# Kernel optimization log

Hardware: AMD Instinct MI355X
Metric: run time of the kernel (lower is better)

Reference implementation:

```python
import jax, jax.numpy as jnp
import numpy as np

B, T, C, HD = 4, 2048, 1024, 64

def setup_inputs() -> dict:
    key = jax.random.key(0)
    kx, kq, kk, kv = jax.random.split(key, 4)
    # Weights stored as [n_embed, head_size]; equivalent to torch Linear weight transposed.
    scale = 1.0 / np.sqrt(C)
    return {
        "x": jax.random.normal(kx, (B, T, C), dtype=jnp.float32),
        "Wq": jax.random.normal(kq, (C, HD), dtype=jnp.float32) * scale,
        "Wk": jax.random.normal(kk, (C, HD), dtype=jnp.float32) * scale,
        "Wv": jax.random.normal(kv, (C, HD), dtype=jnp.float32) * scale,
    }

def reference(x, Wq, Wk, Wv):
    # Projections (no bias)
    q = x @ Wq  # [B,T,HD]
    k = x @ Wk
    v = x @ Wv
    hd = k.shape[-1]
    # NOTE: original multiplies by sqrt(head_size) (not the usual 1/sqrt) -- faithful.
    scores = jnp.einsum("btd,bsd->bts", q, k) * (hd ** 0.5)  # [B,T,T]
    # First softmax over full (unmasked) rows
    w = jax.nn.softmax(scores, axis=-1)
    # Causal mask applied AFTER the first softmax, then a second softmax
    causal = jnp.tril(jnp.ones((q.shape[1], q.shape[1]), dtype=bool))  # [T,T]
    w = jnp.where(causal[None, :, :], w, -jnp.inf)
    w = jax.nn.softmax(w, axis=-1)
    out = jnp.einsum("bts,bsd->btd", w, v)  # [B,T,HD]
    return out
```

## Files before the change

### kernel.cpp

```cpp
#include <hip/hip_runtime.h>
#include <math.h>

#define T_  2048
#define C_  1024
#define HD_ 64

typedef __attribute__((ext_vector_type(8))) short bf16x8;
typedef __attribute__((ext_vector_type(4))) float f32x4;

#define MFMA_BF16(A, B, C) __builtin_amdgcn_mfma_f32_16x16x32_bf16(A, B, C, 0, 0, 0)

__device__ __forceinline__ short f2bf(float f) {
    union { float f; unsigned u; } v; v.f = f;
    unsigned r = v.u + 0x7fffu + ((v.u >> 16) & 1u);
    return (short)(r >> 16);
}
__device__ __forceinline__ float bf2f(short s) {
    union { float f; unsigned u; } v;
    v.u = ((unsigned)(unsigned short)s) << 16;
    return v.f;
}

__global__ __launch_bounds__(256) void prep_w_kernel(
    const float* __restrict__ Wq, const float* __restrict__ Wk,
    const float* __restrict__ Wv, short* __restrict__ wt)
{
    const int m = blockIdx.y;
    const float* W = (m == 0) ? Wq : (m == 1) ? Wk : Wv;
    const int t = threadIdx.x;
    const int c = blockIdx.x * 64 + (t >> 2);
    const int hg = (t & 3) * 16;
    const float4* wp = (const float4*)(W + (size_t)c * HD_ + hg);
    short* hi = wt + (size_t)(m * 2 + 0) * 64 * 1024;
    short* lo = wt + (size_t)(m * 2 + 1) * 64 * 1024;
    #pragma unroll
    for (int u = 0; u < 4; ++u) {
        float4 f = wp[u];
        float vs[4] = {f.x, f.y, f.z, f.w};
        #pragma unroll
        for (int e = 0; e < 4; ++e) {
            int h = hg + u * 4 + e;
            short hh = f2bf(vs[e]);
            hi[(size_t)h * 1024 + c] = hh;
            lo[(size_t)h * 1024 + c] = f2bf(vs[e] - bf2f(hh));
        }
    }
}

__global__ __launch_bounds__(256) void qkv_proj_kernel(
    const float* __restrict__ x, const short* __restrict__ wt,
    short* __restrict__ qhp, short* __restrict__ qlp,
    short* __restrict__ khp, short* __restrict__ klp,
    short* __restrict__ vtp)
{
    __shared__ __align__(16) short xh[32 * 64], xl[32 * 64];
    __shared__ __align__(16) short wh[192 * 64], wl[192 * 64];

    const int t = threadIdx.x, L = t & 63, wv = t >> 6;
    const int R0 = blockIdx.x * 32;
    const int xrow = t >> 3, xch = t & 7;

    f32x4 acc[2][3];
    #pragma unroll
    for (int i = 0; i < 2; ++i)
        #pragma unroll
        for (int j = 0; j < 3; ++j) acc[i][j] = {0.f, 0.f, 0.f, 0.f};

    float4 xa0, xa1;
    bf16x8 wr[2][6];
    const float* xp = x + (size_t)(R0 + xrow) * C_ + xch * 8;

    auto loadX = [&](int c0) {
        xa0 = *(const float4*)(xp + c0);
        xa1 = *(const float4*)(xp + c0 + 4);
    };
    auto loadW = [&](int c0) {
        #pragma unroll
        for (int pl = 0; pl < 2; ++pl)
            #pragma unroll
            for (int u = 0; u < 6; ++u) {
                int cc = t + 256 * u;
                int row = cc >> 3, ch = cc & 7;
                int m = row >> 6, h = row & 63;
                wr[pl][u] = *(const bf16x8*)(wt + (size_t)(m * 2 + pl) * 65536
                                             + (size_t)h * 1024 + c0 + ch * 8);
            }
    };

    loadX(0); loadW(0);
    for (int c0 = 0; c0 < C_; c0 += 64) {
        __syncthreads();
        {
            float vs[8] = {xa0.x, xa0.y, xa0.z, xa0.w, xa1.x, xa1.y, xa1.z, xa1.w};
            bf16x8 vh, vl;
            #pragma unroll
            for (int e = 0; e < 8; ++e) {
                short hh = f2bf(vs[e]);
                vh[e] = hh;
                vl[e] = f2bf(vs[e] - bf2f(hh));
            }
            int slot = (xch ^ (xrow & 7)) * 8;
            *(bf16x8*)&xh[xrow * 64 + slot] = vh;
            *(bf16x8*)&xl[xrow * 64 + slot] = vl;
        }
        {
            #pragma unroll
            for (int pl = 0; pl < 2; ++pl)
                #pragma unroll
                for (int u = 0; u < 6; ++u) {
                    int cc = t + 256 * u;
                    int row = cc >> 3, ch = cc & 7;
                    short* dst = pl ? wl : wh;
                    *(bf16x8*)&dst[row * 64 + ((ch ^ (row & 7)) * 8)] = wr[pl][u];
                }
        }
        if (c0 + 64 < C_) { loadX(c0 + 64); loadW(c0 + 64); }
        __syncthreads();
        #pragma unroll
        for (int kc = 0; kc < 2; ++kc) {
            const int ch = kc * 4 + (L >> 4);
            bf16x8 axh[2], axl[2], bwh[3], bwl[3];
            #pragma unroll
            for (int rt = 0; rt < 2; ++rt) {
                int row = rt * 16 + (L & 15);
                int off = row * 64 + ((ch ^ (row & 7)) * 8);
                axh[rt] = *(const bf16x8*)&xh[off];
                axl[rt] = *(const bf16x8*)&xl[off];
            }
            #pragma unroll
            for (int cl = 0; cl < 3; ++cl) {
                int ct = wv + cl * 4;
                int wrow = ct * 16 + (L & 15);
                int off = wrow * 64 + ((ch ^ (wrow & 7)) * 8);
                bwh[cl] = *(const bf16x8*)&wh[off];
                bwl[cl] = *(const bf16x8*)&wl[off];
            }
            #pragma unroll
            for (int rt = 0; rt < 2; ++rt) {
                acc[rt][0] = MFMA_BF16(axl[rt], bwh[0], acc[rt][0]);
                acc[rt][0] = MFMA_BF16(axh[rt], bwl[0], acc[rt][0]);
                acc[rt][0] = MFMA_BF16(axh[rt], bwh[0], acc[rt][0]);
                acc[rt][1] = MFMA_BF16(axl[rt], bwh[1], acc[rt][1]);
                acc[rt][1] = MFMA_BF16(axh[rt], bwl[1], acc[rt][1]);
                acc[rt][1] = MFMA_BF16(axh[rt], bwh[1], acc[rt][1]);
                acc[rt][2] = MFMA_BF16(bwh[2], axh[rt], acc[rt][2]);
            }
        }
    }

    const int quad = L >> 4;
    #pragma unroll
    for (int rt = 0; rt < 2; ++rt) {
        #pragma unroll
        for (int r = 0; r < 4; ++r) {
            int row = R0 + rt * 16 + quad * 4 + r;
            int h = wv * 16 + (L & 15);
            float vq = acc[rt][0][r] * 8.f;
            short hq = f2bf(vq);
            qhp[(size_t)row * HD_ + h] = hq;
            qlp[(size_t)row * HD_ + h] = f2bf(vq - bf2f(hq));
            float vk = acc[rt][1][r];
            short hk = f2bf(vk);
            khp[(size_t)row * HD_ + h] = hk;
            klp[(size_t)row * HD_ + h] = f2bf(vk - bf2f(hk));
            int d = wv * 16 + quad * 4 + r;
            int tt = R0 + rt * 16 + (L & 15);
            int bb = tt >> 11, tl = tt & (T_ - 1);
            vtp[(size_t)(bb * 64 + d) * T_ + tl] = f2bf(acc[rt][2][r]);
        }
    }
}

__global__ __launch_bounds__(256) void stats_kernel(
    const short* __restrict__ qhp, const short* __restrict__ qlp,
    const short* __restrict__ khp, const short* __restrict__ klp,
    float* __restrict__ pm)
{
    __shared__ __align__(16) short khs[64 * 64], kls[64 * 64];
    __shared__ float red[4 * 64 * 2];

    const int t = threadIdx.x, L = t & 63, wv = t >> 6;
    const int bt = blockIdx.x, seg = blockIdx.y, b = blockIdx.z;
    const int R0 = bt * 64, S0 = seg * 512;

    bf16x8 qfh[4][2], qfl[4][2];
    #pragma unroll
    for (int rt = 0; rt < 4; ++rt)
        #pragma unroll
        for (int dc = 0; dc < 2; ++dc) {
            int row = R0 + rt * 16 + (L & 15);
            size_t off = ((size_t)b * T_ + row) * HD_ + dc * 32 + (L >> 4) * 8;
            qfh[rt][dc] = *(const bf16x8*)(qhp + off);
            qfl[rt][dc] = *(const bf16x8*)(qlp + off);
        }

    float ml[4][4], ll[4][4];
    #pragma unroll
    for (int rt = 0; rt < 4; ++rt)
        #pragma unroll
        for (int r = 0; r < 4; ++r) { ml[rt][r] = -1e30f; ll[rt][r] = 0.f; }

    const int pl = t >> 7, id = t & 127;
    for (int jt = 0; jt < 8; ++jt) {
        __syncthreads();
        {
            const short* src = pl ? klp : khp;
            short* dst = pl ? kls : khs;
            #pragma unroll
            for (int u = 0; u < 4; ++u) {
                int cid = id * 4 + u;
                int col = cid >> 3, ch = cid & 7;
                bf16x8 v = *(const bf16x8*)(src
                    + ((size_t)b * T_ + S0 + jt * 64 + col) * HD_ + ch * 8);
                *(bf16x8*)&dst[col * 64 + ((ch ^ (col & 7)) * 8)] = v;
            }
        }
        __syncthreads();
        const int colL = wv * 16 + (L & 15);
        bf16x8 kf[2], kfl[2];
        #pragma unroll
        for (int dc = 0; dc < 2; ++dc) {
            int ch = dc * 4 + (L >> 4);
            int off = colL * 64 + ((ch ^ (colL & 7)) * 8);
            kf[dc]  = *(const bf16x8*)&khs[off];
            kfl[dc] = *(const bf16x8*)&kls[off];
        }
        #pragma unroll
        for (int rt = 0; rt < 4; ++rt) {
            f32x4 s = {0.f, 0.f, 0.f, 0.f};
            #pragma unroll
            for (int dc = 0; dc < 2; ++dc) {
                s = MFMA_BF16(qfl[rt][dc], kf[dc], s);
                s = MFMA_BF16(qfh[rt][dc], kfl[dc], s);
                s = MFMA_BF16(qfh[rt][dc], kf[dc], s);
            }
            #pragma unroll
            for (int r = 0; r < 4; ++r) {
                float mn = fmaxf(ml[rt][r], s[r]);
                ll[rt][r] = ll[rt][r] * __expf(ml[rt][r] - mn) + __expf(s[r] - mn);
                ml[rt][r] = mn;
            }
        }
    }
    #pragma unroll
    for (int off = 1; off < 16; off <<= 1)
        #pragma unroll
        for (int rt = 0; rt < 4; ++rt)
            #pragma unroll
            for (int r = 0; r < 4; ++r) {
                float mo = __shfl_xor(ml[rt][r], off, 64);
                float lo = __shfl_xor(ll[rt][r], off, 64);
                float mn = fmaxf(ml[rt][r], mo);
                ll[rt][r] = ll[rt][r] * __expf(ml[rt][r] - mn) + lo * __expf(mo - mn);
                ml[rt][r] = mn;
            }
    if ((L & 15) == 0) {
        #pragma unroll
        for (int rt = 0; rt < 4; ++rt)
            #pragma unroll
            for (int r = 0; r < 4; ++r) {
                int row = rt * 16 + (L >> 4) * 4 + r;
                red[(wv * 64 + row) * 2 + 0] = ml[rt][r];
                red[(wv * 64 + row) * 2 + 1] = ll[rt][r];
            }
    }
    __syncthreads();
    if (t < 64) {
        float M = red[t * 2], S = red[t * 2 + 1];
        #pragma unroll
        for (int w = 1; w < 4; ++w) {
            float mo = red[(w * 64 + t) * 2], lo = red[(w * 64 + t) * 2 + 1];
            float mn = fmaxf(M, mo);
            S = S * __expf(M - mn) + lo * __expf(mo - mn);
            M = mn;
        }
        size_t o = ((size_t)((b * 32 + bt) * 4 + seg) * 64 + t) * 2;
        pm[o] = M;
        pm[o + 1] = S;
    }
}

__global__ __launch_bounds__(256) void stat_merge_kernel(
    const float* __restrict__ pm, float* __restrict__ msp, float* __restrict__ ilp)
{
    int gid = blockIdx.x * 256 + threadIdx.x;
    int b = gid >> 11, rl = gid & 2047, bt = rl >> 6, rr = rl & 63;
    float M = -1e30f, S = 0.f;
    #pragma unroll
    for (int seg = 0; seg < 4; ++seg) {
        size_t o = ((size_t)((b * 32 + bt) * 4 + seg) * 64 + rr) * 2;
        float mo = pm[o], lo = pm[o + 1];
        float mn = fmaxf(M, mo);
        S = S * __expf(M - mn) + lo * __expf(mo - mn);
        M = mn;
    }
    msp[gid] = M;
    ilp[gid] = 1.f / S;
}

__global__ __launch_bounds__(512) void pv_kernel(
    const short* __restrict__ qhp, const short* __restrict__ qlp,
    const short* __restrict__ khp, const short* __restrict__ klp,
    const short* __restrict__ vtp, const float* __restrict__ msp,
    const float* __restrict__ ilp, float* __restrict__ out)
{
    __shared__ __align__(16) short khs[128 * 64];
    __shared__ __align__(16) short kls[128 * 64];
    __shared__ __align__(16) short vts[64 * 128];
    __shared__ __align__(16) float es[32 * 128];

    const int t = threadIdx.x, L = t & 63, wv = t >> 6;
    const int b = blockIdx.x >> 6, p = blockIdx.x & 63;
    const int IA = p * 16, IB = (127 - p) * 16;

    bf16x8 qfh[2][2], qfl[2][2];
    #pragma unroll
    for (int rt = 0; rt < 2; ++rt) {
        int row = (rt ? IB : IA) + (L & 15);
        const short* qb  = qhp + ((size_t)b * T_ + row) * HD_;
        const short* qbl = qlp + ((size_t)b * T_ + row) * HD_;
        #pragma unroll
        for (int dc = 0; dc < 2; ++dc) {
            int off = dc * 32 + (L >> 4) * 8;
            qfh[rt][dc] = *(const bf16x8*)(qb + off);
            qfl[rt][dc] = *(const bf16x8*)(qbl + off);
        }
    }
    float ms[2][4], is[2][4];
    int rowg[2][4];
    #pragma unroll
    for (int rt = 0; rt < 2; ++rt)
        #pragma unroll
        for (int r = 0; r < 4; ++r) {
            int rg = (rt ? IB : IA) + (L >> 4) * 4 + r;
            rowg[rt][r] = rg;
            ms[rt][r] = msp[b * T_ + rg];
            is[rt][r] = ilp[b * T_ + rg];
        }

    const short* kbh = khp + (size_t)b * T_ * HD_;
    const short* kbl = klp + (size_t)b * T_ * HD_;
    const short* vb  = vtp + (size_t)b * 64 * T_;
    const int spl = t >> 8, sid = t & 255;

    auto stageK = [&](int jt) {
        const short* src = spl ? kbl : kbh;
        short* dst = spl ? kls : khs;
        #pragma unroll
        for (int u = 0; u < 4; ++u) {
            int cid = sid * 4 + u;
            int col = cid >> 3, c8 = cid & 7;
            bf16x8 v = *(const bf16x8*)(src + (size_t)(jt * 128 + col) * HD_ + c8 * 8);
            *(bf16x8*)&dst[col * 64 + ((c8 ^ (col & 7)) * 8)] = v;
        }
    };
    auto stageV = [&](int jt) {
        #pragma unroll
        for (int u = 0; u < 2; ++u) {
            int cid = t + u * 512;
            int d = cid >> 4, ch = cid & 15;
            bf16x8 v = *(const bf16x8*)(vb + (size_t)d * T_ + jt * 128 + ch * 8);
            *(bf16x8*)&vts[d * 128 + ((ch ^ ((d & 7) * 2)) * 8)] = v;
        }
    };

    const int nA = (IA + 143) >> 7;
    const int nB = (IB + 143) >> 7;
    const int rtp = wv & 1, dh = (wv >> 1) & 1, khf = wv >> 2;
    f32x4 ov[2];
    ov[0] = {0.f, 0.f, 0.f, 0.f};
    ov[1] = {0.f, 0.f, 0.f, 0.f};
    float dn[2][4];
    #pragma unroll
    for (int rt = 0; rt < 2; ++rt)
        #pragma unroll
        for (int r = 0; r < 4; ++r) dn[rt][r] = 0.f;

    for (int jt = 0; jt < nB; ++jt) {
        __syncthreads();
        stageK(jt);
        stageV(jt);
        __syncthreads();
        const int col = wv * 16 + (L & 15);
        bf16x8 kf[2], kfl[2];
        #pragma unroll
        for (int dc = 0; dc < 2; ++dc) {
            int ch = dc * 4 + (L >> 4);
            int off = col * 64 + ((ch ^ (col & 7)) * 8);
            kf[dc]  = *(const bf16x8*)&khs[off];
            kfl[dc] = *(const bf16x8*)&kls[off];
        }
        for (int rt = 0; rt < 2; ++rt) {
            if (rt == 0 && jt >= nA) continue;
            f32x4 s = {0.f, 0.f, 0.f, 0.f};
            #pragma unroll
            for (int dc = 0; dc < 2; ++dc) {
                s = MFMA_BF16(qfl[rt][dc], kf[dc], s);
                s = MFMA_BF16(qfh[rt][dc], kfl[dc], s);
                s = MFMA_BF16(qfh[rt][dc], kf[dc], s);
            }
            #pragma unroll
            for (int r = 0; r < 4; ++r) {
                float pv = __expf(s[r] - ms[rt][r]) * is[rt][r];
                int colg = jt * 128 + col;
                float ev = (colg <= rowg[rt][r]) ? __expf(pv) : 0.f;
                dn[rt][r] += ev;
                int rid = rt * 16 + (L >> 4) * 4 + r;
                es[rid * 128 + (((col >> 3) ^ (rid & 15)) * 8) + (col & 7)] = ev;
            }
        }
        __syncthreads();
        if (!(rtp == 0 && jt >= nA)) {
            #pragma unroll
            for (int u = 0; u < 2; ++u) {
                int kc = khf * 2 + u;
                int rid = rtp * 16 + (L & 15);
                int chunk = (kc * 4 + (L >> 4)) ^ (rid & 15);
                const float* ep = &es[rid * 128 + chunk * 8];
                float4 e0 = *(const float4*)ep;
                float4 e1 = *(const float4*)(ep + 4);
                bf16x8 ef;
                ef[0] = f2bf(e0.x); ef[1] = f2bf(e0.y);
                ef[2] = f2bf(e0.z); ef[3] = f2bf(e0.w);
                ef[4] = f2bf(e1.x); ef[5] = f2bf(e1.y);
                ef[6] = f2bf(e1.z); ef[7] = f2bf(e1.w);
                #pragma unroll
                for (int dt = 0; dt < 2; ++dt) {
                    int d = dh * 32 + dt * 16 + (L & 15);
                    int ch = kc * 4 + (L >> 4);
                    bf16x8 vf = *(const bf16x8*)&vts[d * 128 + ((ch ^ ((d & 7) * 2)) * 8)];
                    ov[dt] = MFMA_BF16(ef, vf, ov[dt]);
                }
            }
        }
    }

    #pragma unroll
    for (int off = 1; off < 16; off <<= 1)
        #pragma unroll
        for (int rt = 0; rt < 2; ++rt)
            #pragma unroll
            for (int r = 0; r < 4; ++r)
                dn[rt][r] += __shfl_xor(dn[rt][r], off, 64);
    __syncthreads();
    float* red  = es + 2304;
    float* dinv = es + 2560;
    if ((L & 15) == 0) {
        #pragma unroll
        for (int rt = 0; rt < 2; ++rt)
            #pragma unroll
            for (int r = 0; r < 4; ++r) {
                int rid = rt * 16 + (L >> 4) * 4 + r;
                red[wv * 32 + rid] = dn[rt][r];
            }
    }
    __syncthreads();
    if (t < 32) {
        float D = 0.f;
        #pragma unroll
        for (int w = 0; w < 8; ++w) D += red[w * 32 + t];
        dinv[t] = 1.f / D;
    }
    float* obuf = es;
    __syncthreads();
    if (khf == 1) {
        #pragma unroll
        for (int dt = 0; dt < 2; ++dt)
            #pragma unroll
            for (int r = 0; r < 4; ++r)
                obuf[((wv - 4) * 64 + L) * 8 + dt * 4 + r] = ov[dt][r];
    }
    __syncthreads();
    if (khf == 0) {
        float* ob = out + (size_t)b * T_ * HD_;
        #pragma unroll
        for (int dt = 0; dt < 2; ++dt)
            #pragma unroll
            for (int r = 0; r < 4; ++r) {
                float o = ov[dt][r] + obuf[(wv * 64 + L) * 8 + dt * 4 + r];
                int rid = rtp * 16 + (L >> 4) * 4 + r;
                int row = (rtp ? IB : IA) + (L >> 4) * 4 + r;
                int d = dh * 32 + dt * 16 + (L & 15);
                ob[(size_t)row * HD_ + d] = o * dinv[rid];
            }
    }
}

extern "C" void kernel_launch(void* const* d_in, const int* in_sizes, int n_in,
                              void* d_out, int out_size, void* d_ws, size_t ws_size,
                              hipStream_t stream) {
    (void)in_sizes; (void)n_in; (void)out_size; (void)ws_size;
    const float* x  = (const float*)d_in[0];
    const float* Wq = (const float*)d_in[1];
    const float* Wk = (const float*)d_in[2];
    const float* Wv = (const float*)d_in[3];
    float* outp = (float*)d_out;

    char* ws = (char*)d_ws;
    short* wt  = (short*)ws;
    float* pm  = (float*)ws;
    float* msp = (float*)(ws + 262144);
    float* ilp = (float*)(ws + 294912);
    short* qh = (short*)(ws + 786432);
    short* ql = (short*)(ws + 786432 + 1048576);
    short* kh = (short*)(ws + 786432 + 2 * 1048576);
    short* kl = (short*)(ws + 786432 + 3 * 1048576);
    short* vt = (short*)(ws + 786432 + 4 * 1048576);

    prep_w_kernel<<<dim3(16, 3), 256, 0, stream>>>(Wq, Wk, Wv, wt);
    qkv_proj_kernel<<<dim3(256), 256, 0, stream>>>(x, wt, qh, ql, kh, kl, vt);
    stats_kernel<<<dim3(32, 4, 4), 256, 0, stream>>>(qh, ql, kh, kl, pm);
    stat_merge_kernel<<<dim3(32), 256, 0, stream>>>(pm, msp, ilp);
    pv_kernel<<<dim3(256), 512, 0, stream>>>(qh, ql, kh, kl, vt, msp, ilp, outp);
}
```

Baseline: 155.8 us.

## Drop LDS staging for K/V/W loads, split-K projection, fuse stats merge

Several independent changes. The weight prep now transposes through LDS so global stores are coalesced. The projection kernel goes to 512 threads, splits the reduction dimension across wave pairs and reads x and weights straight from global memory without LDS tiles, then reduces the partial sums through shared memory. The stats kernel is reorganised so each block owns 16 rows over the full key range, which removes the separate merge kernel and one launch. The pv kernel loads K and V fragments directly from global memory (relying on L2/L1) instead of staging them in swizzled LDS, and uses a padded score buffer. The risk is uncoalesced or repeated global reads in place of the LDS reuse the old code had.

```diff
diff --git a/kernel.cpp b/kernel.cpp
--- a/kernel.cpp
+++ b/kernel.cpp
@@ -25,40 +25,51 @@
     const float* __restrict__ Wq, const float* __restrict__ Wk,
     const float* __restrict__ Wv, short* __restrict__ wt)
 {
+    __shared__ __align__(16) short hi_l[64 * 72], lo_l[64 * 72];
     const int m = blockIdx.y;
     const float* W = (m == 0) ? Wq : (m == 1) ? Wk : Wv;
     const int t = threadIdx.x;
-    const int c = blockIdx.x * 64 + (t >> 2);
-    const int hg = (t & 3) * 16;
-    const float4* wp = (const float4*)(W + (size_t)c * HD_ + hg);
-    short* hi = wt + (size_t)(m * 2 + 0) * 64 * 1024;
-    short* lo = wt + (size_t)(m * 2 + 1) * 64 * 1024;
-    #pragma unroll
-    for (int u = 0; u < 4; ++u) {
-        float4 f = wp[u];
-        float vs[4] = {f.x, f.y, f.z, f.w};
-        #pragma unroll
-        for (int e = 0; e < 4; ++e) {
-            int h = hg + u * 4 + e;
-            short hh = f2bf(vs[e]);
-            hi[(size_t)h * 1024 + c] = hh;
-            lo[(size_t)h * 1024 + c] = f2bf(vs[e] - bf2f(hh));
-        }
-    }
-}
-
-__global__ __launch_bounds__(256) void qkv_proj_kernel(
+    const int C0 = blockIdx.x * 64;
+    {
+        const int c = t >> 2, hq = t & 3;
+        const float4* wp = (const float4*)(W + (size_t)(C0 + c) * HD_ + hq * 16);
+        #pragma unroll
+        for (int u = 0; u < 4; ++u) {
+            float4 f = wp[u];
+            float vs[4] = {f.x, f.y, f.z, f.w};
+            #pragma unroll
+            for (int e = 0; e < 4; ++e) {
+                int h = hq * 16 + u * 4 + e;
+                short hh = f2bf(vs[e]);
+                hi_l[h * 72 + c] = hh;
+                lo_l[h * 72 + c] = f2bf(vs[e] - bf2f(hh));
+            }
+        }
+    }
+    __syncthreads();
+    {
+        const int h = t >> 2, cc = (t & 3) * 16;
+        short* dh = wt + (size_t)(m * 2 + 0) * 65536 + h * 1024 + C0 + cc;
+        short* dl = wt + (size_t)(m * 2 + 1) * 65536 + h * 1024 + C0 + cc;
+        *(bf16x8*)dh       = *(const bf16x8*)&hi_l[h * 72 + cc];
+        *(bf16x8*)(dh + 8) = *(const bf16x8*)&hi_l[h * 72 + cc + 8];
+        *(bf16x8*)dl       = *(const bf16x8*)&lo_l[h * 72 + cc];
+        *(bf16x8*)(dl + 8) = *(const bf16x8*)&lo_l[h * 72 + cc + 8];
+    }
+}
+
+__global__ __launch_bounds__(512) void qkv_proj_kernel(
     const float* __restrict__ x, const short* __restrict__ wt,
     short* __restrict__ qhp, short* __restrict__ qlp,
     short* __restrict__ khp, short* __restrict__ klp,
     short* __restrict__ vtp)
 {
-    __shared__ __align__(16) short xh[32 * 64], xl[32 * 64];
-    __shared__ __align__(16) short wh[192 * 64], wl[192 * 64];
+    __shared__ __align__(16) float pbuf[4 * 64 * 28];
 
     const int t = threadIdx.x, L = t & 63, wv = t >> 6;
+    const int kq = wv & 1, colq = wv >> 1;
     const int R0 = blockIdx.x * 32;
-    const int xrow = t >> 3, xch = t & 7;
+    const int h = colq * 16 + (L & 15);
 
     f32x4 acc[2][3];
     #pragma unroll
@@ -66,107 +77,81 @@
         #pragma unroll
         for (int j = 0; j < 3; ++j) acc[i][j] = {0.f, 0.f, 0.f, 0.f};
 
-    float4 xa0, xa1;
-    bf16x8 wr[2][6];
-    const float* xp = x + (size_t)(R0 + xrow) * C_ + xch * 8;
-
-    auto loadX = [&](int c0) {
-        xa0 = *(const float4*)(xp + c0);
-        xa1 = *(const float4*)(xp + c0 + 4);
-    };
-    auto loadW = [&](int c0) {
-        #pragma unroll
-        for (int pl = 0; pl < 2; ++pl)
-            #pragma unroll
-            for (int u = 0; u < 6; ++u) {
-                int cc = t + 256 * u;
-                int row = cc >> 3, ch = cc & 7;
-                int m = row >> 6, h = row & 63;
-                wr[pl][u] = *(const bf16x8*)(wt + (size_t)(m * 2 + pl) * 65536
-                                             + (size_t)h * 1024 + c0 + ch * 8);
-            }
-    };
-
-    loadX(0); loadW(0);
-    for (int c0 = 0; c0 < C_; c0 += 64) {
-        __syncthreads();
-        {
-            float vs[8] = {xa0.x, xa0.y, xa0.z, xa0.w, xa1.x, xa1.y, xa1.z, xa1.w};
-            bf16x8 vh, vl;
+    const int c_base = kq * 512 + (L >> 4) * 8;
+    const float* xp0 = x + (size_t)(R0 + (L & 15)) * C_ + c_base;
+    const float* xp1 = x + (size_t)(R0 + 16 + (L & 15)) * C_ + c_base;
+    const short* wq_h = wt + (size_t)0 * 65536 + h * 1024 + c_base;
+    const short* wq_l = wt + (size_t)1 * 65536 + h * 1024 + c_base;
+    const short* wk_h = wt + (size_t)2 * 65536 + h * 1024 + c_base;
+    const short* wk_l = wt + (size_t)3 * 65536 + h * 1024 + c_base;
+    const short* wv_h = wt + (size_t)4 * 65536 + h * 1024 + c_base;
+
+    for (int it = 0; it < 16; ++it) {
+        const int c0 = it * 32;
+        bf16x8 axh[2], axl[2];
+        #pragma unroll
+        for (int rt = 0; rt < 2; ++rt) {
+            const float* xp = rt ? xp1 : xp0;
+            float4 f0 = *(const float4*)(xp + c0);
+            float4 f1 = *(const float4*)(xp + c0 + 4);
+            float vs[8] = {f0.x, f0.y, f0.z, f0.w, f1.x, f1.y, f1.z, f1.w};
             #pragma unroll
             for (int e = 0; e < 8; ++e) {
                 short hh = f2bf(vs[e]);
-                vh[e] = hh;
-                vl[e] = f2bf(vs[e] - bf2f(hh));
-            }
-            int slot = (xch ^ (xrow & 7)) * 8;
-            *(bf16x8*)&xh[xrow * 64 + slot] = vh;
-            *(bf16x8*)&xl[xrow * 64 + slot] = vl;
-        }
-        {
-            #pragma unroll
-            for (int pl = 0; pl < 2; ++pl)
-                #pragma unroll
-                for (int u = 0; u < 6; ++u) {
-                    int cc = t + 256 * u;
-                    int row = cc >> 3, ch = cc & 7;
-                    short* dst = pl ? wl : wh;
-                    *(bf16x8*)&dst[row * 64 + ((ch ^ (row & 7)) * 8)] = wr[pl][u];
-                }
-        }
-        if (c0 + 64 < C_) { loadX(c0 + 64); loadW(c0 + 64); }
-        __syncthreads();
-        #pragma unroll
-        for (int kc = 0; kc < 2; ++kc) {
-            const int ch = kc * 4 + (L >> 4);
-            bf16x8 axh[2], axl[2], bwh[3], bwl[3];
-            #pragma unroll
-            for (int rt = 0; rt < 2; ++rt) {
-                int row = rt * 16 + (L & 15);
-                int off = row * 64 + ((ch ^ (row & 7)) * 8);
-                axh[rt] = *(const bf16x8*)&xh[off];
-                axl[rt] = *(const bf16x8*)&xl[off];
-            }
-            #pragma unroll
-            for (int cl = 0; cl < 3; ++cl) {
-                int ct = wv + cl * 4;
-                int wrow = ct * 16 + (L & 15);
-                int off = wrow * 64 + ((ch ^ (wrow & 7)) * 8);
-                bwh[cl] = *(const bf16x8*)&wh[off];
-                bwl[cl] = *(const bf16x8*)&wl[off];
-            }
-            #pragma unroll
-            for (int rt = 0; rt < 2; ++rt) {
-                acc[rt][0] = MFMA_BF16(axl[rt], bwh[0], acc[rt][0]);
-                acc[rt][0] = MFMA_BF16(axh[rt], bwl[0], acc[rt][0]);
-                acc[rt][0] = MFMA_BF16(axh[rt], bwh[0], acc[rt][0]);
-                acc[rt][1] = MFMA_BF16(axl[rt], bwh[1], acc[rt][1]);
-                acc[rt][1] = MFMA_BF16(axh[rt], bwl[1], acc[rt][1]);
-                acc[rt][1] = MFMA_BF16(axh[rt], bwh[1], acc[rt][1]);
-                acc[rt][2] = MFMA_BF16(bwh[2], axh[rt], acc[rt][2]);
-            }
-        }
-    }
-
-    const int quad = L >> 4;
-    #pragma unroll
-    for (int rt = 0; rt < 2; ++rt) {
-        #pragma unroll
-        for (int r = 0; r < 4; ++r) {
-            int row = R0 + rt * 16 + quad * 4 + r;
-            int h = wv * 16 + (L & 15);
-            float vq = acc[rt][0][r] * 8.f;
-            short hq = f2bf(vq);
-            qhp[(size_t)row * HD_ + h] = hq;
-            qlp[(size_t)row * HD_ + h] = f2bf(vq - bf2f(hq));
-            float vk = acc[rt][1][r];
-            short hk = f2bf(vk);
-            khp[(size_t)row * HD_ + h] = hk;
-            klp[(size_t)row * HD_ + h] = f2bf(vk - bf2f(hk));
-            int d = wv * 16 + quad * 4 + r;
-            int tt = R0 + rt * 16 + (L & 15);
-            int bb = tt >> 11, tl = tt & (T_ - 1);
-            vtp[(size_t)(bb * 64 + d) * T_ + tl] = f2bf(acc[rt][2][r]);
+                axh[rt][e] = hh;
+                axl[rt][e] = f2bf(vs[e] - bf2f(hh));
+            }
+        }
+        bf16x8 qh_f = *(const bf16x8*)(wq_h + c0);
+        bf16x8 ql_f = *(const bf16x8*)(wq_l + c0);
+        bf16x8 kh_f = *(const bf16x8*)(wk_h + c0);
+        bf16x8 kl_f = *(const bf16x8*)(wk_l + c0);
+        bf16x8 vh_f = *(const bf16x8*)(wv_h + c0);
+        #pragma unroll
+        for (int rt = 0; rt < 2; ++rt) {
+            acc[rt][0] = MFMA_BF16(axl[rt], qh_f, acc[rt][0]);
+            acc[rt][0] = MFMA_BF16(axh[rt], ql_f, acc[rt][0]);
+            acc[rt][0] = MFMA_BF16(axh[rt], qh_f, acc[rt][0]);
+            acc[rt][1] = MFMA_BF16(axl[rt], kh_f, acc[rt][1]);
+            acc[rt][1] = MFMA_BF16(axh[rt], kl_f, acc[rt][1]);
+            acc[rt][1] = MFMA_BF16(axh[rt], kh_f, acc[rt][1]);
+            acc[rt][2] = MFMA_BF16(vh_f, axh[rt], acc[rt][2]);
+        }
+    }
+
+    if (kq == 1) {
+        float* pb = &pbuf[(colq * 64 + L) * 28];
+        #pragma unroll
+        for (int rt = 0; rt < 2; ++rt)
+            #pragma unroll
+            for (int j = 0; j < 3; ++j)
+                *(f32x4*)&pb[(rt * 3 + j) * 4] = acc[rt][j];
+    }
+    __syncthreads();
+    if (kq == 0) {
+        const float* pb = &pbuf[(colq * 64 + L) * 28];
+        const int quad = L >> 4;
+        #pragma unroll
+        for (int rt = 0; rt < 2; ++rt) {
+            f32x4 aq = acc[rt][0] + *(const f32x4*)&pb[(rt * 3 + 0) * 4];
+            f32x4 ak = acc[rt][1] + *(const f32x4*)&pb[(rt * 3 + 1) * 4];
+            f32x4 av = acc[rt][2] + *(const f32x4*)&pb[(rt * 3 + 2) * 4];
+            #pragma unroll
+            for (int r = 0; r < 4; ++r) {
+                int row = R0 + rt * 16 + quad * 4 + r;
+                float vq = aq[r] * 8.f;
+                short hq2 = f2bf(vq);
+                qhp[(size_t)row * HD_ + h] = hq2;
+                qlp[(size_t)row * HD_ + h] = f2bf(vq - bf2f(hq2));
+                float vk = ak[r];
+                short hk2 = f2bf(vk);
+                khp[(size_t)row * HD_ + h] = hk2;
+                klp[(size_t)row * HD_ + h] = f2bf(vk - bf2f(hk2));
+                int d = colq * 16 + quad * 4 + r;
+                int tt = R0 + rt * 16 + (L & 15);
+                int bb = tt >> 11, tl = tt & (T_ - 1);
+                vtp[(size_t)(bb * 64 + d) * T_ + tl] = f2bf(av[r]);
+            }
         }
     }
 }
@@ -174,128 +159,93 @@
 __global__ __launch_bounds__(256) void stats_kernel(
     const short* __restrict__ qhp, const short* __restrict__ qlp,
     const short* __restrict__ khp, const short* __restrict__ klp,
-    float* __restrict__ pm)
+    float* __restrict__ msp, float* __restrict__ ilp)
 {
-    __shared__ __align__(16) short khs[64 * 64], kls[64 * 64];
-    __shared__ float red[4 * 64 * 2];
+    __shared__ float smem[4][16][2];
 
     const int t = threadIdx.x, L = t & 63, wv = t >> 6;
-    const int bt = blockIdx.x, seg = blockIdx.y, b = blockIdx.z;
-    const int R0 = bt * 64, S0 = seg * 512;
-
-    bf16x8 qfh[4][2], qfl[4][2];
-    #pragma unroll
-    for (int rt = 0; rt < 4; ++rt)
+    const int R0 = blockIdx.x * 16;
+    const int b = R0 >> 11;
+    const int CB = (b << 11) + wv * 512;
+
+    bf16x8 qfh[2], qfl[2];
+    {
+        int row = R0 + (L & 15);
         #pragma unroll
         for (int dc = 0; dc < 2; ++dc) {
-            int row = R0 + rt * 16 + (L & 15);
-            size_t off = ((size_t)b * T_ + row) * HD_ + dc * 32 + (L >> 4) * 8;
-            qfh[rt][dc] = *(const bf16x8*)(qhp + off);
-            qfl[rt][dc] = *(const bf16x8*)(qlp + off);
-        }
-
-    float ml[4][4], ll[4][4];
-    #pragma unroll
-    for (int rt = 0; rt < 4; ++rt)
-        #pragma unroll
-        for (int r = 0; r < 4; ++r) { ml[rt][r] = -1e30f; ll[rt][r] = 0.f; }
-
-    const int pl = t >> 7, id = t & 127;
-    for (int jt = 0; jt < 8; ++jt) {
-        __syncthreads();
-        {
-            const short* src = pl ? klp : khp;
-            short* dst = pl ? kls : khs;
-            #pragma unroll
-            for (int u = 0; u < 4; ++u) {
-                int cid = id * 4 + u;
-                int col = cid >> 3, ch = cid & 7;
-                bf16x8 v = *(const bf16x8*)(src
-                    + ((size_t)b * T_ + S0 + jt * 64 + col) * HD_ + ch * 8);
-                *(bf16x8*)&dst[col * 64 + ((ch ^ (col & 7)) * 8)] = v;
-            }
-        }
-        __syncthreads();
-        const int colL = wv * 16 + (L & 15);
-        bf16x8 kf[2], kfl[2];
-        #pragma unroll
-        for (int dc = 0; dc < 2; ++dc) {
-            int ch = dc * 4 + (L >> 4);
-            int off = colL * 64 + ((ch ^ (colL & 7)) * 8);
-            kf[dc]  = *(const bf16x8*)&khs[off];
-            kfl[dc] = *(const bf16x8*)&kls[off];
-        }
-        #pragma unroll
-        for (int rt = 0; rt < 4; ++rt) {
-            f32x4 s = {0.f, 0.f, 0.f, 0.f};
-            #pragma unroll
-            for (int dc = 0; dc < 2; ++dc) {
-                s = MFMA_BF16(qfl[rt][dc], kf[dc], s);
-                s = MFMA_BF16(qfh[rt][dc], kfl[dc], s);
-                s = MFMA_BF16(qfh[rt][dc], kf[dc], s);
-            }
-            #pragma unroll
-            for (int r = 0; r < 4; ++r) {
-                float mn = fmaxf(ml[rt][r], s[r]);
-                ll[rt][r] = ll[rt][r] * __expf(ml[rt][r] - mn) + __expf(s[r] - mn);
-                ml[rt][r] = mn;
-            }
+            size_t off = (size_t)row * HD_ + dc * 32 + (L >> 4) * 8;
+            qfh[dc] = *(const bf16x8*)(qhp + off);
+            qfl[dc] = *(const bf16x8*)(qlp + off);
+        }
+    }
+
+    float M[4], S[4];
+    #pragma unroll
+    for (int r = 0; r < 4; ++r) { M[r] = -1e30f; S[r] = 0.f; }
+
+    for (int chunk = 0; chunk < 2; ++chunk) {
+        f32x4 s[16];
+        #pragma unroll
+        for (int ct = 0; ct < 16; ++ct) {
+            int col = CB + (chunk * 16 + ct) * 16 + (L & 15);
+            const short* kb  = khp + (size_t)col * HD_ + (L >> 4) * 8;
+            const short* kb2 = klp + (size_t)col * HD_ + (L >> 4) * 8;
+            bf16x8 kf0 = *(const bf16x8*)kb;
+            bf16x8 kf1 = *(const bf16x8*)(kb + 32);
+            bf16x8 kl0 = *(const bf16x8*)kb2;
+            bf16x8 kl1 = *(const bf16x8*)(kb2 + 32);
+            f32x4 a = {0.f, 0.f, 0.f, 0.f};
+            a = MFMA_BF16(qfl[0], kf0, a);
+            a = MFMA_BF16(qfh[0], kl0, a);
+            a = MFMA_BF16(qfh[0], kf0, a);
+            a = MFMA_BF16(qfl[1], kf1, a);
+            a = MFMA_BF16(qfh[1], kl1, a);
+            a = MFMA_BF16(qfh[1], kf1, a);
+            s[ct] = a;
+        }
+        #pragma unroll
+        for (int r = 0; r < 4; ++r) {
+            float mc = s[0][r];
+            #pragma unroll
+            for (int ct = 1; ct < 16; ++ct) mc = fmaxf(mc, s[ct][r]);
+            float lc = 0.f;
+            #pragma unroll
+            for (int ct = 0; ct < 16; ++ct) lc += __expf(s[ct][r] - mc);
+            float mn = fmaxf(M[r], mc);
+            S[r] = S[r] * __expf(M[r] - mn) + lc * __expf(mc - mn);
+            M[r] = mn;
         }
     }
     #pragma unroll
     for (int off = 1; off < 16; off <<= 1)
         #pragma unroll
-        for (int rt = 0; rt < 4; ++rt)
-            #pragma unroll
-            for (int r = 0; r < 4; ++r) {
-                float mo = __shfl_xor(ml[rt][r], off, 64);
-                float lo = __shfl_xor(ll[rt][r], off, 64);
-                float mn = fmaxf(ml[rt][r], mo);
-                ll[rt][r] = ll[rt][r] * __expf(ml[rt][r] - mn) + lo * __expf(mo - mn);
-                ml[rt][r] = mn;
-            }
+        for (int r = 0; r < 4; ++r) {
+            float mo = __shfl_xor(M[r], off, 64);
+            float lo = __shfl_xor(S[r], off, 64);
+            float mn = fmaxf(M[r], mo);
+            S[r] = S[r] * __expf(M[r] - mn) + lo * __expf(mo - mn);
+            M[r] = mn;
+        }
     if ((L & 15) == 0) {
         #pragma unroll
-        for (int rt = 0; rt < 4; ++rt)
-            #pragma unroll
-            for (int r = 0; r < 4; ++r) {
-                int row = rt * 16 + (L >> 4) * 4 + r;
-                red[(wv * 64 + row) * 2 + 0] = ml[rt][r];
-                red[(wv * 64 + row) * 2 + 1] = ll[rt][r];
-            }
-    }
-    __syncthreads();
-    if (t < 64) {
-        float M = red[t * 2], S = red[t * 2 + 1];
+        for (int r = 0; r < 4; ++r) {
+            smem[wv][(L >> 4) * 4 + r][0] = M[r];
+            smem[wv][(L >> 4) * 4 + r][1] = S[r];
+        }
+    }
+    __syncthreads();
+    if (t < 16) {
+        float Mm = smem[0][t][0], Ss = smem[0][t][1];
         #pragma unroll
         for (int w = 1; w < 4; ++w) {
-            float mo = red[(w * 64 + t) * 2], lo = red[(w * 64 + t) * 2 + 1];
-            float mn = fmaxf(M, mo);
-            S = S * __expf(M - mn) + lo * __expf(mo - mn);
-            M = mn;
-        }
-        size_t o = ((size_t)((b * 32 + bt) * 4 + seg) * 64 + t) * 2;
-        pm[o] = M;
-        pm[o + 1] = S;
-    }
-}
-
-__global__ __launch_bounds__(256) void stat_merge_kernel(
-    const float* __restrict__ pm, float* __restrict__ msp, float* __restrict__ ilp)
-{
-    int gid = blockIdx.x * 256 + threadIdx.x;
-    int b = gid >> 11, rl = gid & 2047, bt = rl >> 6, rr = rl & 63;
-    float M = -1e30f, S = 0.f;
-    #pragma unroll
-    for (int seg = 0; seg < 4; ++seg) {
-        size_t o = ((size_t)((b * 32 + bt) * 4 + seg) * 64 + rr) * 2;
-        float mo = pm[o], lo = pm[o + 1];
-        float mn = fmaxf(M, mo);
-        S = S * __expf(M - mn) + lo * __expf(mo - mn);
-        M = mn;
-    }
-    msp[gid] = M;
-    ilp[gid] = 1.f / S;
+            float mo = smem[w][t][0], lo = smem[w][t][1];
+            float mn = fmaxf(Mm, mo);
+            Ss = Ss * __expf(Mm - mn) + lo * __expf(mo - mn);
+            Mm = mn;
+        }
+        msp[R0 + t] = Mm;
+        ilp[R0 + t] = 1.f / Ss;
+    }
 }
 
 __global__ __launch_bounds__(512) void pv_kernel(
@@ -304,10 +254,10 @@
     const short* __restrict__ vtp, const float* __restrict__ msp,
     const float* __restrict__ ilp, float* __restrict__ out)
 {
-    __shared__ __align__(16) short khs[128 * 64];
-    __shared__ __align__(16) short kls[128 * 64];
-    __shared__ __align__(16) short vts[64 * 128];
-    __shared__ __align__(16) float es[32 * 128];
+    __shared__ __align__(16) float es[32 * 132];
+    __shared__ float red[8 * 32];
+    __shared__ float dinv[32];
+    __shared__ float obuf[4 * 64 * 8];
 
     const int t = threadIdx.x, L = t & 63, wv = t >> 6;
     const int b = blockIdx.x >> 6, p = blockIdx.x & 63;
@@ -317,8 +267,8 @@
     #pragma unroll
     for (int rt = 0; rt < 2; ++rt) {
         int row = (rt ? IB : IA) + (L & 15);
-        const short* qb  = qhp + ((size_t)b * T_ + row) * HD_;
-        const short* qbl = qlp + ((size_t)b * T_ + row) * HD_;
+        const short* qb  = qhp + ((size_t)(b << 11) + row) * HD_;
+        const short* qbl = qlp + ((size_t)(b << 11) + row) * HD_;
         #pragma unroll
         for (int dc = 0; dc < 2; ++dc) {
             int off = dc * 32 + (L >> 4) * 8;
@@ -334,35 +284,9 @@
         for (int r = 0; r < 4; ++r) {
             int rg = (rt ? IB : IA) + (L >> 4) * 4 + r;
             rowg[rt][r] = rg;
-            ms[rt][r] = msp[b * T_ + rg];
-            is[rt][r] = ilp[b * T_ + rg];
-        }
-
-    const short* kbh = khp + (size_t)b * T_ * HD_;
-    const short* kbl = klp + (size_t)b * T_ * HD_;
-    const short* vb  = vtp + (size_t)b * 64 * T_;
-    const int spl = t >> 8, sid = t & 255;
-
-    auto stageK = [&](int jt) {
-        const short* src = spl ? kbl : kbh;
-        short* dst = spl ? kls : khs;
-        #pragma unroll
-        for (int u = 0; u < 4; ++u) {
-            int cid = sid * 4 + u;
-            int col = cid >> 3, c8 = cid & 7;
-            bf16x8 v = *(const bf16x8*)(src + (size_t)(jt * 128 + col) * HD_ + c8 * 8);
-            *(bf16x8*)&dst[col * 64 + ((c8 ^ (col & 7)) * 8)] = v;
-        }
-    };
-    auto stageV = [&](int jt) {
-        #pragma unroll
-        for (int u = 0; u < 2; ++u) {
-            int cid = t + u * 512;
-            int d = cid >> 4, ch = cid & 15;
-            bf16x8 v = *(const bf16x8*)(vb + (size_t)d * T_ + jt * 128 + ch * 8);
-            *(bf16x8*)&vts[d * 128 + ((ch ^ ((d & 7) * 2)) * 8)] = v;
-        }
-    };
+            ms[rt][r] = msp[(b << 11) + rg];
+            is[rt][r] = ilp[(b << 11) + rg];
+        }
 
     const int nA = (IA + 143) >> 7;
     const int nB = (IB + 143) >> 7;
@@ -378,45 +302,40 @@
 
     for (int jt = 0; jt < nB; ++jt) {
         __syncthreads();
-        stageK(jt);
-        stageV(jt);
-        __syncthreads();
-        const int col = wv * 16 + (L & 15);
-        bf16x8 kf[2], kfl[2];
-        #pragma unroll
-        for (int dc = 0; dc < 2; ++dc) {
-            int ch = dc * 4 + (L >> 4);
-            int off = col * 64 + ((ch ^ (col & 7)) * 8);
-            kf[dc]  = *(const bf16x8*)&khs[off];
-            kfl[dc] = *(const bf16x8*)&kls[off];
-        }
+        const int colL = wv * 16 + (L & 15);
+        const int gcol = (b << 11) + jt * 128 + colL;
+        const short* kb  = khp + (size_t)gcol * HD_ + (L >> 4) * 8;
+        const short* kb2 = klp + (size_t)gcol * HD_ + (L >> 4) * 8;
+        bf16x8 kf0 = *(const bf16x8*)kb;
+        bf16x8 kf1 = *(const bf16x8*)(kb + 32);
+        bf16x8 kl0 = *(const bf16x8*)kb2;
+        bf16x8 kl1 = *(const bf16x8*)(kb2 + 32);
         for (int rt = 0; rt < 2; ++rt) {
             if (rt == 0 && jt >= nA) continue;
             f32x4 s = {0.f, 0.f, 0.f, 0.f};
-            #pragma unroll
-            for (int dc = 0; dc < 2; ++dc) {
-                s = MFMA_BF16(qfl[rt][dc], kf[dc], s);
-                s = MFMA_BF16(qfh[rt][dc], kfl[dc], s);
-                s = MFMA_BF16(qfh[rt][dc], kf[dc], s);
-            }
+            s = MFMA_BF16(qfl[rt][0], kf0, s);
+            s = MFMA_BF16(qfh[rt][0], kl0, s);
+            s = MFMA_BF16(qfh[rt][0], kf0, s);
+            s = MFMA_BF16(qfl[rt][1], kf1, s);
+            s = MFMA_BF16(qfh[rt][1], kl1, s);
+            s = MFMA_BF16(qfh[rt][1], kf1, s);
+            const int colg = jt * 128 + colL;
             #pragma unroll
             for (int r = 0; r < 4; ++r) {
                 float pv = __expf(s[r] - ms[rt][r]) * is[rt][r];
-                int colg = jt * 128 + col;
                 float ev = (colg <= rowg[rt][r]) ? __expf(pv) : 0.f;
                 dn[rt][r] += ev;
                 int rid = rt * 16 + (L >> 4) * 4 + r;
-                es[rid * 128 + (((col >> 3) ^ (rid & 15)) * 8) + (col & 7)] = ev;
+                es[rid * 132 + colL] = ev;
             }
         }
         __syncthreads();
         if (!(rtp == 0 && jt >= nA)) {
             #pragma unroll
             for (int u = 0; u < 2; ++u) {
-                int kc = khf * 2 + u;
-                int rid = rtp * 16 + (L & 15);
-                int chunk = (kc * 4 + (L >> 4)) ^ (rid & 15);
-                const float* ep = &es[rid * 128 + chunk * 8];
+                const int kc = khf * 2 + u;
+                const int rid = rtp * 16 + (L & 15);
+                const float* ep = &es[rid * 132 + kc * 32 + (L >> 4) * 8];
                 float4 e0 = *(const float4*)ep;
                 float4 e1 = *(const float4*)(ep + 4);
                 bf16x8 ef;
@@ -427,8 +346,9 @@
                 #pragma unroll
                 for (int dt = 0; dt < 2; ++dt) {
                     int d = dh * 32 + dt * 16 + (L & 15);
-                    int ch = kc * 4 + (L >> 4);
-                    bf16x8 vf = *(const bf16x8*)&vts[d * 128 + ((ch ^ ((d & 7) * 2)) * 8)];
+                    const short* vp = vtp + ((size_t)(b * 64 + d) << 11)
+                                    + jt * 128 + kc * 32 + (L >> 4) * 8;
+                    bf16x8 vf = *(const bf16x8*)vp;
                     ov[dt] = MFMA_BF16(ef, vf, ov[dt]);
                 }
             }
@@ -442,9 +362,6 @@
             #pragma unroll
             for (int r = 0; r < 4; ++r)
                 dn[rt][r] += __shfl_xor(dn[rt][r], off, 64);
-    __syncthreads();
-    float* red  = es + 2304;
-    float* dinv = es + 2560;
     if ((L & 15) == 0) {
         #pragma unroll
         for (int rt = 0; rt < 2; ++rt)
@@ -461,7 +378,6 @@
         for (int w = 0; w < 8; ++w) D += red[w * 32 + t];
         dinv[t] = 1.f / D;
     }
-    float* obuf = es;
     __syncthreads();
     if (khf == 1) {
         #pragma unroll
@@ -472,7 +388,7 @@
     }
     __syncthreads();
     if (khf == 0) {
-        float* ob = out + (size_t)b * T_ * HD_;
+        float* ob = out + (size_t)(b << 11) * HD_;
         #pragma unroll
         for (int dt = 0; dt < 2; ++dt)
             #pragma unroll
@@ -498,9 +414,8 @@
 
     char* ws = (char*)d_ws;
     short* wt  = (short*)ws;
-    float* pm  = (float*)ws;
-    float* msp = (float*)(ws + 262144);
-    float* ilp = (float*)(ws + 294912);
+    float* msp = (float*)ws;
+    float* ilp = (float*)(ws + 32768);
     short* qh = (short*)(ws + 786432);
     short* ql = (short*)(ws + 786432 + 1048576);
     short* kh = (short*)(ws + 786432 + 2 * 1048576);
@@ -508,8 +423,7 @@
     short* vt = (short*)(ws + 786432 + 4 * 1048576);
 
     prep_w_kernel<<<dim3(16, 3), 256, 0, stream>>>(Wq, Wk, Wv, wt);
-    qkv_proj_kernel<<<dim3(256), 256, 0, stream>>>(x, wt, qh, ql, kh, kl, vt);
-    stats_kernel<<<dim3(32, 4, 4), 256, 0, stream>>>(qh, ql, kh, kl, pm);
-    stat_merge_kernel<<<dim3(32), 256, 0, stream>>>(pm, msp, ilp);
+    qkv_proj_kernel<<<dim3(256), 512, 0, stream>>>(x, wt, qh, ql, kh, kl, vt);
+    stats_kernel<<<dim3(512), 256, 0, stream>>>(qh, ql, kh, kl, msp, ilp);
     pv_kernel<<<dim3(256), 512, 0, stream>>>(qh, ql, kh, kl, vt, msp, ilp, outp);
 }
```

Result: slower. 183.7 us (+17.9%).
